# Performance work log

Hardware: AMD Instinct MI355X
Metric: run time of the kernel (lower is better)

Reference implementation:

```python
import jax, jax.numpy as jnp
import numpy as np

N = 100000   # nodes
E = 1600000  # edges
G = 256      # graphs in batch
IN = 128     # in_feats
H = 64       # h_feats


def _xavier(k, shape):
    fan_in, fan_out = shape
    lim = float(np.sqrt(6.0 / (fan_in + fan_out)))
    return jax.random.uniform(k, shape, jnp.float32, -lim, lim)


def setup_inputs() -> dict:
    key = jax.random.key(0)
    ks = jax.random.split(key, 12)
    x = jax.random.normal(ks[0], (N, IN), jnp.float32)
    src = jax.random.randint(ks[1], (E,), 0, N)
    dst = jax.random.randint(ks[2], (E,), 0, N)
    ew = jax.random.uniform(ks[3], (E,), jnp.float32)
    gid = jnp.sort(jax.random.randint(ks[4], (N,), 0, G))
    def lin(k, fi, fo):
        kw, kb = jax.random.split(k)
        lim = float(np.sqrt(1.0 / fi))
        return (jax.random.uniform(kw, (fi, fo), jnp.float32, -lim, lim),
                jax.random.uniform(kb, (fo,), jnp.float32, -lim, lim))
    W1 = _xavier(ks[5], (IN, H)); b1 = jnp.zeros((H,), jnp.float32)
    W2 = _xavier(ks[6], (H, H));  b2 = jnp.zeros((H,), jnp.float32)
    W3 = _xavier(ks[7], (H, H));  b3 = jnp.zeros((H,), jnp.float32)
    Dw1, Db1 = lin(ks[8], H, 16)
    Dw2, Db2 = lin(ks[9], 16, 8)
    Dw3, Db3 = lin(ks[10], 8, 1)
    return {"x": x, "src": src, "dst": dst, "ew": ew, "gid": gid,
            "W1": W1, "b1": b1, "W2": W2, "b2": b2, "W3": W3, "b3": b3,
            "Dw1": Dw1, "Db1": Db1, "Dw2": Dw2, "Db2": Db2, "Dw3": Dw3, "Db3": Db3}


def reference(x, src, dst, ew, gid, W1, b1, W2, b2, W3, b3,
              Dw1, Db1, Dw2, Db2, Dw3, Db3):
    n = x.shape[0]
    # DGL GraphConv norm='both': unweighted degrees, clamped to >= 1
    deg_out = jnp.zeros((n,), x.dtype).at[src].add(1.0)
    deg_in = jnp.zeros((n,), x.dtype).at[dst].add(1.0)
    ns = jax.lax.rsqrt(jnp.maximum(deg_out, 1.0))  # src-side norm
    nd = jax.lax.rsqrt(jnp.maximum(deg_in, 1.0))   # dst-side norm

    def conv(h, W, b):
        # apply weight first (in >= out), then gather-scale-scatter
        h = (h * ns[:, None]) @ W                      # [N, out]
        m = h[src] * ew[:, None]                       # [E, out] edge messages
        agg = jnp.zeros((n, W.shape[1]), h.dtype).at[dst].add(m)
        return agg * nd[:, None] + b

    h = jax.nn.relu(conv(x, W1, b1))
    h = jax.nn.relu(conv(h, W2, b2))
    h = jax.nn.relu(conv(h, W3, b3))

    # mean_nodes: per-graph mean pooling
    counts = jnp.zeros((G,), h.dtype).at[gid].add(1.0)
    pooled = jnp.zeros((G, h.shape[1]), h.dtype).at[gid].add(h)
    pooled = pooled / jnp.maximum(counts, 1.0)[:, None]

    h = jax.nn.relu(pooled @ Dw1 + Db1)
    h = jax.nn.relu(h @ Dw2 + Db2)
    return jax.nn.sigmoid(h @ Dw3 + Db3)  # [G, 1]
```

## Files before the change

kernel.cpp:

```cpp
#include <hip/hip_runtime.h>
#include <math.h>

#define N_NODES 100000
#define N_EDGES 1600000
#define G_GRAPHS 256
#define IN_F 128
#define H_F 64

#define HB 20
#define HCHUNK (N_EDGES / HB)
#define NWORDS (N_NODES / 4)
#define HNODES 25000
#define HWORDS (HNODES / 4)
#define HR 4

#define NREG 160
#define REG_NODES 625
#define BUCKET_CAP 11000
#define BSPAN 6400
#define NB_BUCKET (N_EDGES / BSPAN)
#define RSLACK 1280
#define STG_CAP 12880
#define CSR_ALLOC 1806336

typedef unsigned int uint_t;
typedef unsigned short ushort_t;
typedef unsigned char uchar_t;
typedef __attribute__((ext_vector_type(8))) short short8;
typedef __attribute__((ext_vector_type(4))) float floatx4;
typedef __attribute__((ext_vector_type(2))) float floatx2;

__device__ __forceinline__ ushort_t f2bf(float f) {
  uint_t u = __float_as_uint(f);
  uint_t r = (u + 0x7fffu + ((u >> 16) & 1u)) >> 16;
  return (ushort_t)r;
}
__device__ __forceinline__ float bflo(uint_t u) { return __uint_as_float(u << 16); }
__device__ __forceinline__ uchar_t f2fp8(float f) {
  return (uchar_t)(__builtin_amdgcn_cvt_pk_fp8_f32(f, f, 0, false) & 0xff);
}
__device__ __forceinline__ int sw_idx(int row, int kshort) {
  int slot = kshort >> 3;
  return row * 64 + (((slot ^ (row & 7)) << 3) | (kshort & 7));
}

__global__ __launch_bounds__(256) void build_a_kernel(
    const int* __restrict__ src, const int* __restrict__ dst,
    const float* __restrict__ ew, int* __restrict__ bcnt,
    uint2* __restrict__ bucket, uint_t* __restrict__ p8src) {
  __shared__ uint_t shm[BSPAN + 2 * NREG];
  if (blockIdx.x < NB_BUCKET) {
    uint_t* rl = shm;
    int* cnt = (int*)(shm + BSPAN);
    int* cur = cnt + NREG;
    const int e0 = blockIdx.x * BSPAN;

    for (int i = threadIdx.x; i < NREG; i += 256) cnt[i] = 0;
    __syncthreads();

    for (int i = threadIdx.x; i < BSPAN; i += 256) {
      uint_t d = (uint_t)dst[e0 + i];
      uint_t r = d / REG_NODES;
      uint_t loc = d - r * REG_NODES;
      rl[i] = (r << 16) | loc;
      atomicAdd(&cnt[r], 1);
    }
    __syncthreads();

    for (int i = threadIdx.x; i < NREG; i += 256)
      cur[i] = atomicAdd(&bcnt[i], cnt[i]);
    __syncthreads();

    for (int i = threadIdx.x; i < BSPAN; i += 256) {
      uint_t v = rl[i];
      uint_t r = v >> 16, loc = v & 0xffffu;
      int pos = atomicAdd(&cur[r], 1);
      if (pos < BUCKET_CAP)
        bucket[(size_t)r * BUCKET_CAP + pos] = make_uint2(
            (loc << 17) | (uint_t)src[e0 + i], __float_as_uint(ew[e0 + i]));
    }
  } else {
    uint_t* h = shm;
    const int idx = blockIdx.x - NB_BUCKET;
    const int r = idx / HB;
    const int b = idx % HB;
    const uint_t rbase = (uint_t)(r * HNODES);

    for (int i = threadIdx.x; i < HWORDS; i += 256) h[i] = 0u;
    __syncthreads();

    const uint4* k4 = (const uint4*)(src + b * HCHUNK);
    for (int i = threadIdx.x; i < HCHUNK / 4; i += 256) {
      uint4 v = k4[i];
      uint_t t;
      t = v.x - rbase; if (t < (uint_t)HNODES) atomicAdd(&h[t >> 2], 1u << ((t & 3u) * 8u));
      t = v.y - rbase; if (t < (uint_t)HNODES) atomicAdd(&h[t >> 2], 1u << ((t & 3u) * 8u));
      t = v.z - rbase; if (t < (uint_t)HNODES) atomicAdd(&h[t >> 2], 1u << ((t & 3u) * 8u));
      t = v.w - rbase; if (t < (uint_t)HNODES) atomicAdd(&h[t >> 2], 1u << ((t & 3u) * 8u));
    }
    __syncthreads();

    uint_t* outp = p8src + (size_t)b * NWORDS + r * HWORDS;
    for (int i = threadIdx.x; i < HWORDS; i += 256) outp[i] = h[i];
  }
}

__global__ __launch_bounds__(1024) void build_b_kernel(
    const uint2* __restrict__ bucket, const int* __restrict__ bcnt,
    const uint_t* __restrict__ p8src, uint_t* __restrict__ csr,
    int2* __restrict__ rc, float* __restrict__ nd, float* __restrict__ ns) {
  __shared__ uint_t staged[STG_CAP];
  __shared__ int cnt[REG_NODES];
  __shared__ int sc[REG_NODES];
  __shared__ int ts[1024];
  const int tid = threadIdx.x;
  if (blockIdx.x >= NREG) {
    int w = (blockIdx.x - NREG) * 1024 + tid;
    if (w >= NWORDS) return;
    int c0 = 0, c1 = 0, c2 = 0, c3 = 0;
    for (int b = 0; b < HB; ++b) {
      uint_t xv = p8src[(size_t)b * NWORDS + w];
      c0 += (int)(xv & 0xffu);
      c1 += (int)((xv >> 8) & 0xffu);
      c2 += (int)((xv >> 16) & 0xffu);
      c3 += (int)((xv >> 24) & 0xffu);
    }
    ((float4*)ns)[w] = make_float4(
        rsqrtf(fmaxf((float)c0, 1.0f)), rsqrtf(fmaxf((float)c1, 1.0f)),
        rsqrtf(fmaxf((float)c2, 1.0f)), rsqrtf(fmaxf((float)c3, 1.0f)));
    return;
  }
  const int r = blockIdx.x;
  const int nE = min(bcnt[r], BUCKET_CAP);
  const int alloc_r = ((nE + 3) & ~3) + RSLACK;

  ts[tid] = (tid < NREG) ? (((min(bcnt[tid], BUCKET_CAP) + 3) & ~3) + RSLACK) : 0;
  for (int i = tid; i < REG_NODES; i += 1024) cnt[i] = 0;
  __syncthreads();
  for (int off = 1; off < 256; off <<= 1) {
    int t = (tid >= off) ? ts[tid - off] : 0;
    __syncthreads();
    ts[tid] += t;
    __syncthreads();
  }
  const int csr_base = (r == 0) ? 0 : ts[r - 1];
  __syncthreads();

  const uint2* bk = bucket + (size_t)r * BUCKET_CAP;
  for (int i = tid; i < nE; i += 1024) atomicAdd(&cnt[bk[i].x >> 17], 1);
  __syncthreads();

  int cv = (tid < REG_NODES) ? cnt[tid] : 0;
  int pv = (cv + 3) & ~3;
  ts[tid] = pv;
  __syncthreads();
  for (int off = 1; off < 1024; off <<= 1) {
    int t = (tid >= off) ? ts[tid - off] : 0;
    __syncthreads();
    ts[tid] += t;
    __syncthreads();
  }
  if (tid < REG_NODES) {
    int run = (tid == 0) ? 0 : ts[tid - 1];
    sc[tid] = run;
    int v = r * REG_NODES + tid;
    rc[v] = make_int2(csr_base + run, cv);
    nd[v] = rsqrtf(fmaxf((float)cv, 1.0f));
  }
  __syncthreads();
  const int ptot = min(ts[1023], STG_CAP);
  __syncthreads();

  for (int i = tid; i < ptot; i += 1024) staged[i] = 0u;
  __syncthreads();

  for (int i = tid; i < nE; i += 1024) {
    uint2 e = bk[i];
    uint_t loc = e.x >> 17;
    int pos = atomicAdd(&sc[loc], 1);
    if (pos < STG_CAP)
      staged[pos] = ((uint_t)(f2bf(__uint_as_float(e.y)) & 0x7fff) << 17) |
                    (e.x & 0x1ffffu);
  }
  __syncthreads();

  const int out_len = min(ptot, alloc_r);
  for (int i = tid; i < out_len; i += 1024) csr[csr_base + i] = staged[i];
}

template <int K, bool AFP32>
__global__ __launch_bounds__(256) void gemm_mfma_kernel(
    const void* __restrict__ Xin, const float* __restrict__ W,
    const float* __restrict__ ns, uchar_t* __restrict__ T, int ntiles) {
  constexpr int CH = K / 32;
  constexpr int WROW = K + 8;
  __shared__ __align__(16) ushort_t Wt[64 * WROW];
  const int tid = threadIdx.x;

  for (int i = tid; i < K * 64; i += 256) {
    int k = i >> 6, nn = i & 63;
    Wt[nn * WROW + k] = f2bf(W[i]);
  }
  __syncthreads();

  const int wave = tid >> 6;
  const int lane = tid & 63;
  const int tile = blockIdx.x * 4 + wave;
  if (tile >= ntiles) return;
  const int m = lane & 15;
  const int q = lane >> 4;
  const int node0 = tile * 16;

  short8 afrag[CH];
  if (AFP32) {
    const float* xr = (const float*)Xin + (size_t)(node0 + m) * K + q * 8;
#pragma unroll
    for (int c = 0; c < CH; ++c) {
      float4 xa = *(const float4*)(xr + c * 32);
      float4 xb = *(const float4*)(xr + c * 32 + 4);
      short8 a;
      a[0] = (short)f2bf(xa.x); a[1] = (short)f2bf(xa.y);
      a[2] = (short)f2bf(xa.z); a[3] = (short)f2bf(xa.w);
      a[4] = (short)f2bf(xb.x); a[5] = (short)f2bf(xb.y);
      a[6] = (short)f2bf(xb.z); a[7] = (short)f2bf(xb.w);
      afrag[c] = a;
    }
  } else {
    const ushort_t* xr = (const ushort_t*)Xin + (size_t)(node0 + m) * K + q * 8;
#pragma unroll
    for (int c = 0; c < CH; ++c)
      afrag[c] = *(const short8*)(xr + c * 32);
  }

  floatx4 acc[4];
#pragma unroll
  for (int t = 0; t < 4; ++t) acc[t] = (floatx4){0.f, 0.f, 0.f, 0.f};

#pragma unroll
  for (int t = 0; t < 4; ++t) {
    const ushort_t* wr = &Wt[(t * 16 + m) * WROW + q * 8];
#pragma unroll
    for (int c = 0; c < CH; ++c) {
      short8 bfrag = *(const short8*)(wr + c * 32);
      acc[t] = __builtin_amdgcn_mfma_f32_16x16x32_bf16(afrag[c], bfrag, acc[t], 0, 0, 0);
    }
  }

  float4 nsv = *(const float4*)(ns + node0 + q * 4);
  const float nsa[4] = {nsv.x, nsv.y, nsv.z, nsv.w};
#pragma unroll
  for (int t = 0; t < 4; ++t) {
#pragma unroll
    for (int r = 0; r < 4; ++r) {
      int node = node0 + q * 4 + r;
      T[(size_t)node * 64 + t * 16 + m] = f2fp8(acc[t][r] * nsa[r]);
    }
  }
}

__device__ __forceinline__ void gacc1(float acc[8], uint_t e, uint2 p) {
  float w = __uint_as_float((e >> 17) << 16);
  floatx2 a;
  a = __builtin_amdgcn_cvt_pk_f32_fp8(p.x, false);
  acc[0] = fmaf(a.x, w, acc[0]); acc[1] = fmaf(a.y, w, acc[1]);
  a = __builtin_amdgcn_cvt_pk_f32_fp8(p.x, true);
  acc[2] = fmaf(a.x, w, acc[2]); acc[3] = fmaf(a.y, w, acc[3]);
  a = __builtin_amdgcn_cvt_pk_f32_fp8(p.y, false);
  acc[4] = fmaf(a.x, w, acc[4]); acc[5] = fmaf(a.y, w, acc[5]);
  a = __builtin_amdgcn_cvt_pk_f32_fp8(p.y, true);
  acc[6] = fmaf(a.x, w, acc[6]); acc[7] = fmaf(a.y, w, acc[7]);
}

template <bool POOL>
__global__ __launch_bounds__(256, 6) void fused_kernel(
    const uint_t* __restrict__ csr, const int2* __restrict__ rc,
    const uchar_t* __restrict__ T, const float* __restrict__ nd,
    const float* __restrict__ bias, const float* __restrict__ ns,
    const float* __restrict__ W, uchar_t* __restrict__ Tout,
    const int* __restrict__ gid, float* __restrict__ pooled) {
  __shared__ __align__(16) ushort_t Hs[POOL ? 8 : 64 * 64];
  __shared__ __align__(16) ushort_t Wt[POOL ? 8 : 64 * 64];
  __shared__ float gaccF[POOL ? 4 * 64 : 1];
  __shared__ int g0s;
  const int tid = threadIdx.x;
  const int node_base = blockIdx.x * 64;

  if constexpr (POOL) {
    gaccF[tid] = 0.0f;
    if (tid == 0) g0s = gid[node_base];
  } else {
    for (int i = tid; i < H_F * 64; i += 256) {
      int k = i >> 6, nn = i & 63;
      Wt[sw_idx(nn, k)] = f2bf(W[i]);
    }
  }
  __syncthreads();

  const int lane = tid & 63;
  const int wv = tid >> 6;
  const int o = lane >> 3, l = lane & 7;
  const uint2* Tp = (const uint2*)T;

  const float4 b0 = *(const float4*)&bias[l * 8];
  const float4 b1v = *(const float4*)&bias[l * 8 + 4];

#pragma unroll 1
  for (int pass = 0; pass < 2; ++pass) {
    const int ln = pass * 32 + wv * 8 + o;
    const int v = node_base + ln;
    if (v < N_NODES) {
      int2 rcv = rc[v];
      const uint4* c4 = (const uint4*)(csr + rcv.x);
      const int nb4 = (rcv.y + 3) >> 2;

      float acc[8] = {0, 0, 0, 0, 0, 0, 0, 0};
      int kq = 0;
      for (; kq + 2 <= nb4; kq += 2) {
        uint4 ea = c4[kq];
        uint4 eb = c4[kq + 1];
        uint2 p0 = Tp[(size_t)(ea.x & 0x1ffffu) * 8 + l];
        uint2 p1 = Tp[(size_t)(ea.y & 0x1ffffu) * 8 + l];
        uint2 p2 = Tp[(size_t)(ea.z & 0x1ffffu) * 8 + l];
        uint2 p3 = Tp[(size_t)(ea.w & 0x1ffffu) * 8 + l];
        uint2 p4 = Tp[(size_t)(eb.x & 0x1ffffu) * 8 + l];
        uint2 p5 = Tp[(size_t)(eb.y & 0x1ffffu) * 8 + l];
        uint2 p6 = Tp[(size_t)(eb.z & 0x1ffffu) * 8 + l];
        uint2 p7 = Tp[(size_t)(eb.w & 0x1ffffu) * 8 + l];
        gacc1(acc, ea.x, p0); gacc1(acc, ea.y, p1);
        gacc1(acc, ea.z, p2); gacc1(acc, ea.w, p3);
        gacc1(acc, eb.x, p4); gacc1(acc, eb.y, p5);
        gacc1(acc, eb.z, p6); gacc1(acc, eb.w, p7);
      }
      if (kq < nb4) {
        uint4 ea = c4[kq];
        uint2 p0 = Tp[(size_t)(ea.x & 0x1ffffu) * 8 + l];
        uint2 p1 = Tp[(size_t)(ea.y & 0x1ffffu) * 8 + l];
        uint2 p2 = Tp[(size_t)(ea.z & 0x1ffffu) * 8 + l];
        uint2 p3 = Tp[(size_t)(ea.w & 0x1ffffu) * 8 + l];
        gacc1(acc, ea.x, p0); gacc1(acc, ea.y, p1);
        gacc1(acc, ea.z, p2); gacc1(acc, ea.w, p3);
      }

      const float ndv = nd[v];
      if constexpr (!POOL) {
        uint4 ov;
        ov.x = (uint_t)f2bf(fmaxf(fmaf(acc[0], ndv, b0.x), 0.f)) |
               ((uint_t)f2bf(fmaxf(fmaf(acc[1], ndv, b0.y), 0.f)) << 16);
        ov.y = (uint_t)f2bf(fmaxf(fmaf(acc[2], ndv, b0.z), 0.f)) |
               ((uint_t)f2bf(fmaxf(fmaf(acc[3], ndv, b0.w), 0.f)) << 16);
        ov.z = (uint_t)f2bf(fmaxf(fmaf(acc[4], ndv, b1v.x), 0.f)) |
               ((uint_t)f2bf(fmaxf(fmaf(acc[5], ndv, b1v.y), 0.f)) << 16);
        ov.w = (uint_t)f2bf(fmaxf(fmaf(acc[6], ndv, b1v.z), 0.f)) |
               ((uint_t)f2bf(fmaxf(fmaf(acc[7], ndv, b1v.w), 0.f)) << 16);
        *((uint4*)&Hs[sw_idx(ln, l * 8)]) = ov;
      } else {
        const float bb[8] = {b0.x, b0.y, b0.z, b0.w, b1v.x, b1v.y, b1v.z, b1v.w};
        float vals[8];
#pragma unroll
        for (int f = 0; f < 8; ++f)
          vals[f] = bflo((uint_t)f2bf(fmaxf(fmaf(acc[f], ndv, bb[f]), 0.f)));
        int g = gid[v];
        int gl = g - g0s;
        if (gl >= 0 && gl < 4) {
#pragma unroll
          for (int f = 0; f < 8; ++f)
            atomicAdd(&gaccF[gl * 64 + l * 8 + f], vals[f]);
        } else {
#pragma unroll
          for (int f = 0; f < 8; ++f)
            atomicAdd(&pooled[(size_t)g * 64 + l * 8 + f], vals[f]);
        }
      }
    }
  }
  __syncthreads();

  if constexpr (!POOL) {
    const int m = lane & 15, q = lane >> 4;
    const int node0 = node_base + wv * 16;
    if (node0 < N_NODES) {
      short8 afrag[2];
      afrag[0] = *(const short8*)&Hs[sw_idx(wv * 16 + m, q * 8)];
      afrag[1] = *(const short8*)&Hs[sw_idx(wv * 16 + m, q * 8 + 32)];

      floatx4 acc4v[4];
#pragma unroll
      for (int t = 0; t < 4; ++t) acc4v[t] = (floatx4){0.f, 0.f, 0.f, 0.f};
#pragma unroll
      for (int t = 0; t < 4; ++t) {
#pragma unroll
        for (int c = 0; c < 2; ++c) {
          short8 bfrag = *(const short8*)&Wt[sw_idx(t * 16 + m, q * 8 + c * 32)];
          acc4v[t] = __builtin_amdgcn_mfma_f32_16x16x32_bf16(afrag[c], bfrag,
                                                            acc4v[t], 0, 0, 0);
        }
      }
      float4 nsv = *(const float4*)(ns + node0 + q * 4);
      const float nsa[4] = {nsv.x, nsv.y, nsv.z, nsv.w};
#pragma unroll
      for (int t = 0; t < 4; ++t) {
#pragma unroll
        for (int r2 = 0; r2 < 4; ++r2) {
          int node = node0 + q * 4 + r2;
          Tout[(size_t)node * 64 + t * 16 + m] = f2fp8(acc4v[t][r2] * nsa[r2]);
        }
      }
    }
  } else {
    int vlast = node_base + 63;
    if (vlast >= N_NODES) vlast = N_NODES - 1;
    int span = gid[vlast] - g0s + 1;
    if (span > 4) span = 4;
    if (tid < span * 64) {
      int gl = tid >> 6, j = tid & 63;
      int g = g0s + gl;
      if (g < G_GRAPHS) {
        float vsum = gaccF[gl * 64 + j];
        if (vsum != 0.0f) atomicAdd(&pooled[(size_t)g * 64 + j], vsum);
      }
    }
  }
}

__global__ __launch_bounds__(256) void pool_mlp_kernel(
    const float* __restrict__ pooled, const int* __restrict__ gid,
    const float* __restrict__ Dw1, const float* __restrict__ Db1,
    const float* __restrict__ Dw2, const float* __restrict__ Db2,
    const float* __restrict__ Dw3, const float* __restrict__ Db3,
    float* __restrict__ out) {
  __shared__ float mean[64];
  __shared__ float h1s[16], h2s[8];
  const int g = blockIdx.x;
  int l = 0, r = N_NODES;
  while (l < r) { int m = (l + r) >> 1; if (gid[m] < g) l = m + 1; else r = m; }
  const int lo = l;
  r = N_NODES;
  while (l < r) { int m = (l + r) >> 1; if (gid[m] < g + 1) l = m + 1; else r = m; }
  const int hi = l;

  if (threadIdx.x < 64) {
    float inv = 1.0f / fmaxf((float)(hi - lo), 1.0f);
    mean[threadIdx.x] = pooled[(size_t)g * 64 + threadIdx.x] * inv;
  }
  __syncthreads();
  if (threadIdx.x < 16) {
    int o = threadIdx.x;
    float a = Db1[o];
#pragma unroll
    for (int k = 0; k < 64; ++k) a = fmaf(mean[k], Dw1[k * 16 + o], a);
    h1s[o] = fmaxf(a, 0.0f);
  }
  __syncthreads();
  if (threadIdx.x < 8) {
    int o = threadIdx.x;
    float a = Db2[o];
#pragma unroll
    for (int k = 0; k < 16; ++k) a = fmaf(h1s[k], Dw2[k * 8 + o], a);
    h2s[o] = fmaxf(a, 0.0f);
  }
  __syncthreads();
  if (threadIdx.x == 0) {
    float a = Db3[0];
#pragma unroll
    for (int k = 0; k < 8; ++k) a = fmaf(h2s[k], Dw3[k], a);
    out[g] = 1.0f / (1.0f + expf(-a));
  }
}

extern "C" void kernel_launch(void* const* d_in, const int* in_sizes, int n_in,
                              void* d_out, int out_size, void* d_ws, size_t ws_size,
                              hipStream_t stream) {
  const float* x   = (const float*)d_in[0];
  const int*   src = (const int*)  d_in[1];
  const int*   dst = (const int*)  d_in[2];
  const float* ew  = (const float*)d_in[3];
  const int*   gid = (const int*)  d_in[4];
  const float* W1  = (const float*)d_in[5];
  const float* b1  = (const float*)d_in[6];
  const float* W2  = (const float*)d_in[7];
  const float* b2  = (const float*)d_in[8];
  const float* W3  = (const float*)d_in[9];
  const float* b3  = (const float*)d_in[10];
  const float* Dw1 = (const float*)d_in[11];
  const float* Db1 = (const float*)d_in[12];
  const float* Dw2 = (const float*)d_in[13];
  const float* Db2 = (const float*)d_in[14];
  const float* Dw3 = (const float*)d_in[15];
  const float* Db3 = (const float*)d_in[16];
  float* out = (float*)d_out;

  char* ws = (char*)d_ws;
  const size_t TSZ = (size_t)N_NODES * 64;
  const size_t BUCKET_BYTES = (size_t)NREG * BUCKET_CAP * 8;
  uchar_t*  T_a   = (uchar_t*)ws;
  uchar_t*  T_b   = (uchar_t*)(ws + TSZ);
  uint2*    bucket = (uint2*)ws;
  char* p = ws + BUCKET_BYTES;
  uint_t*   csr   = (uint_t*)p;          p += (size_t)CSR_ALLOC * 4;
  uint_t*   p8src = (uint_t*)p;          p += (size_t)HB * NWORDS * 4;
  float*    ns    = (float*)p;           p += (size_t)N_NODES * 4;
  float*    nd    = (float*)p;           p += (size_t)N_NODES * 4;
  int2*     rc    = (int2*)p;            p += (size_t)N_NODES * 8;
  int*      bcnt  = (int*)p;             p += (size_t)NREG * 4;
  float*    pooled = (float*)p;

  const int NTILES  = N_NODES / 16;
  const int NB_A    = NB_BUCKET + HR * HB;
  const int NB_B    = NREG + (NWORDS + 1023) / 1024;
  const int NB_GEMM = (NTILES + 3) / 4;
  const int NB_F    = (N_NODES + 63) / 64;

  hipMemsetAsync(bcnt, 0,
                 NREG * sizeof(int) + G_GRAPHS * H_F * sizeof(float), stream);
  build_a_kernel<<<NB_A, 256, 0, stream>>>(src, dst, ew, bcnt, bucket, p8src);
  build_b_kernel<<<NB_B, 1024, 0, stream>>>(bucket, bcnt, p8src, csr, rc, nd, ns);

  gemm_mfma_kernel<IN_F, true><<<NB_GEMM, 256, 0, stream>>>(x, W1, ns, T_a, NTILES);
  fused_kernel<false><<<NB_F, 256, 0, stream>>>(csr, rc, T_a, nd, b1, ns, W2,
                                                T_b, nullptr, nullptr);
  fused_kernel<false><<<NB_F, 256, 0, stream>>>(csr, rc, T_b, nd, b2, ns, W3,
                                                T_a, nullptr, nullptr);
  fused_kernel<true><<<NB_F, 256, 0, stream>>>(csr, rc, T_a, nd, b3, nullptr,
                                               nullptr, nullptr, gid, pooled);

  pool_mlp_kernel<<<G_GRAPHS, 256, 0, stream>>>(pooled, gid, Dw1, Db1, Dw2, Db2,
                                                Dw3, Db3, out);
}
```

Before: 289.2 us.

## Switch aggregation to edge-balanced work split with packed CSR and LDS accumulation

The per-node aggregation loop is replaced with an edge-parallel scheme. Each block walks the contiguous edge range of its 64 nodes. Octets of lanes process 8 edges each, receive edge descriptors through ds_bpermute, and flush run-length partial sums into an LDS accumulator with atomics. The CSR drops the per-node padding to multiples of 4 and gains a byte array holding each edge's local destination index. The aim is to remove load imbalance from skewed degrees and the wasted padding traffic, at the cost of LDS atomics, an extra byte stream per edge, and lower occupancy (launch bound 4 instead of 6).

```diff
diff --git a/kernel.cpp b/kernel.cpp
--- a/kernel.cpp
+++ b/kernel.cpp
@@ -19,9 +19,7 @@
 #define BUCKET_CAP 11000
 #define BSPAN 6400
 #define NB_BUCKET (N_EDGES / BSPAN)
-#define RSLACK 1280
-#define STG_CAP 12880
-#define CSR_ALLOC 1806336
+#define CSR_SLACK 512
 
 typedef unsigned int uint_t;
 typedef unsigned short ushort_t;
@@ -108,8 +106,10 @@
 __global__ __launch_bounds__(1024) void build_b_kernel(
     const uint2* __restrict__ bucket, const int* __restrict__ bcnt,
     const uint_t* __restrict__ p8src, uint_t* __restrict__ csr,
-    int2* __restrict__ rc, float* __restrict__ nd, float* __restrict__ ns) {
-  __shared__ uint_t staged[STG_CAP];
+    uchar_t* __restrict__ locb, int2* __restrict__ rc,
+    float* __restrict__ nd, float* __restrict__ ns) {
+  __shared__ uint_t staged[BUCKET_CAP];
+  __shared__ uchar_t stagedb[BUCKET_CAP];
   __shared__ int cnt[REG_NODES];
   __shared__ int sc[REG_NODES];
   __shared__ int ts[1024];
@@ -132,9 +132,8 @@
   }
   const int r = blockIdx.x;
   const int nE = min(bcnt[r], BUCKET_CAP);
-  const int alloc_r = ((nE + 3) & ~3) + RSLACK;
-
-  ts[tid] = (tid < NREG) ? (((min(bcnt[tid], BUCKET_CAP) + 3) & ~3) + RSLACK) : 0;
+
+  ts[tid] = (tid < NREG) ? min(bcnt[tid], BUCKET_CAP) : 0;
   for (int i = tid; i < REG_NODES; i += 1024) cnt[i] = 0;
   __syncthreads();
   for (int off = 1; off < 256; off <<= 1) {
@@ -151,8 +150,7 @@
   __syncthreads();
 
   int cv = (tid < REG_NODES) ? cnt[tid] : 0;
-  int pv = (cv + 3) & ~3;
-  ts[tid] = pv;
+  ts[tid] = cv;
   __syncthreads();
   for (int off = 1; off < 1024; off <<= 1) {
     int t = (tid >= off) ? ts[tid - off] : 0;
@@ -168,24 +166,21 @@
     nd[v] = rsqrtf(fmaxf((float)cv, 1.0f));
   }
   __syncthreads();
-  const int ptot = min(ts[1023], STG_CAP);
-  __syncthreads();
-
-  for (int i = tid; i < ptot; i += 1024) staged[i] = 0u;
-  __syncthreads();
 
   for (int i = tid; i < nE; i += 1024) {
     uint2 e = bk[i];
     uint_t loc = e.x >> 17;
     int pos = atomicAdd(&sc[loc], 1);
-    if (pos < STG_CAP)
-      staged[pos] = ((uint_t)(f2bf(__uint_as_float(e.y)) & 0x7fff) << 17) |
-                    (e.x & 0x1ffffu);
-  }
-  __syncthreads();
-
-  const int out_len = min(ptot, alloc_r);
-  for (int i = tid; i < out_len; i += 1024) csr[csr_base + i] = staged[i];
+    staged[pos] = ((uint_t)(f2bf(__uint_as_float(e.y)) & 0x7fff) << 17) |
+                  (e.x & 0x1ffffu);
+    stagedb[pos] = (uchar_t)(((uint_t)r * REG_NODES + loc) & 63u);
+  }
+  __syncthreads();
+
+  for (int i = tid; i < nE; i += 1024) {
+    csr[csr_base + i] = staged[i];
+    locb[csr_base + i] = stagedb[i];
+  }
 }
 
 template <int K, bool AFP32>
@@ -258,33 +253,23 @@
   }
 }
 
-__device__ __forceinline__ void gacc1(float acc[8], uint_t e, uint2 p) {
-  float w = __uint_as_float((e >> 17) << 16);
-  floatx2 a;
-  a = __builtin_amdgcn_cvt_pk_f32_fp8(p.x, false);
-  acc[0] = fmaf(a.x, w, acc[0]); acc[1] = fmaf(a.y, w, acc[1]);
-  a = __builtin_amdgcn_cvt_pk_f32_fp8(p.x, true);
-  acc[2] = fmaf(a.x, w, acc[2]); acc[3] = fmaf(a.y, w, acc[3]);
-  a = __builtin_amdgcn_cvt_pk_f32_fp8(p.y, false);
-  acc[4] = fmaf(a.x, w, acc[4]); acc[5] = fmaf(a.y, w, acc[5]);
-  a = __builtin_amdgcn_cvt_pk_f32_fp8(p.y, true);
-  acc[6] = fmaf(a.x, w, acc[6]); acc[7] = fmaf(a.y, w, acc[7]);
-}
-
 template <bool POOL>
-__global__ __launch_bounds__(256, 6) void fused_kernel(
-    const uint_t* __restrict__ csr, const int2* __restrict__ rc,
-    const uchar_t* __restrict__ T, const float* __restrict__ nd,
-    const float* __restrict__ bias, const float* __restrict__ ns,
-    const float* __restrict__ W, uchar_t* __restrict__ Tout,
-    const int* __restrict__ gid, float* __restrict__ pooled) {
-  __shared__ __align__(16) ushort_t Hs[POOL ? 8 : 64 * 64];
+__global__ __launch_bounds__(256, 4) void fused_kernel(
+    const uint_t* __restrict__ csr, const uchar_t* __restrict__ locb,
+    const int2* __restrict__ rc, const uchar_t* __restrict__ T,
+    const float* __restrict__ nd, const float* __restrict__ bias,
+    const float* __restrict__ ns, const float* __restrict__ W,
+    uchar_t* __restrict__ Tout, const int* __restrict__ gid,
+    float* __restrict__ pooled) {
+  __shared__ float Hacc[64 * 65];
   __shared__ __align__(16) ushort_t Wt[POOL ? 8 : 64 * 64];
-  __shared__ float gaccF[POOL ? 4 * 64 : 1];
+  __shared__ float gaccF[POOL ? 256 : 1];
   __shared__ int g0s;
   const int tid = threadIdx.x;
   const int node_base = blockIdx.x * 64;
-
+  const int vlast = min(node_base + 63, N_NODES - 1);
+
+  for (int i = tid; i < 64 * 65; i += 256) Hacc[i] = 0.0f;
   if constexpr (POOL) {
     gaccF[tid] = 0.0f;
     if (tid == 0) g0s = gid[node_base];
@@ -299,78 +284,73 @@
   const int lane = tid & 63;
   const int wv = tid >> 6;
   const int o = lane >> 3, l = lane & 7;
+  const int oct = wv * 8 + o;
   const uint2* Tp = (const uint2*)T;
 
-  const float4 b0 = *(const float4*)&bias[l * 8];
-  const float4 b1v = *(const float4*)&bias[l * 8 + 4];
-
-#pragma unroll 1
-  for (int pass = 0; pass < 2; ++pass) {
-    const int ln = pass * 32 + wv * 8 + o;
-    const int v = node_base + ln;
-    if (v < N_NODES) {
-      int2 rcv = rc[v];
-      const uint4* c4 = (const uint4*)(csr + rcv.x);
-      const int nb4 = (rcv.y + 3) >> 2;
-
-      float acc[8] = {0, 0, 0, 0, 0, 0, 0, 0};
-      int kq = 0;
-      for (; kq + 2 <= nb4; kq += 2) {
-        uint4 ea = c4[kq];
-        uint4 eb = c4[kq + 1];
-        uint2 p0 = Tp[(size_t)(ea.x & 0x1ffffu) * 8 + l];
-        uint2 p1 = Tp[(size_t)(ea.y & 0x1ffffu) * 8 + l];
-        uint2 p2 = Tp[(size_t)(ea.z & 0x1ffffu) * 8 + l];
-        uint2 p3 = Tp[(size_t)(ea.w & 0x1ffffu) * 8 + l];
-        uint2 p4 = Tp[(size_t)(eb.x & 0x1ffffu) * 8 + l];
-        uint2 p5 = Tp[(size_t)(eb.y & 0x1ffffu) * 8 + l];
-        uint2 p6 = Tp[(size_t)(eb.z & 0x1ffffu) * 8 + l];
-        uint2 p7 = Tp[(size_t)(eb.w & 0x1ffffu) * 8 + l];
-        gacc1(acc, ea.x, p0); gacc1(acc, ea.y, p1);
-        gacc1(acc, ea.z, p2); gacc1(acc, ea.w, p3);
-        gacc1(acc, eb.x, p4); gacc1(acc, eb.y, p5);
-        gacc1(acc, eb.z, p6); gacc1(acc, eb.w, p7);
+  const int2 rc0 = rc[node_base];
+  const int2 rcL = rc[vlast];
+  const int ws = rc0.x;
+  const int we = rcL.x + rcL.y;
+
+  float acc[8] = {0, 0, 0, 0, 0, 0, 0, 0};
+  int loc_run = -1;
+
+  int eb = ws + oct * 8;
+  if (eb < we) {
+    uint_t dl = csr[eb + l];
+    uint_t bl = (uint_t)locb[eb + l];
+    for (; eb < we; eb += 256) {
+      uint_t dln = csr[eb + 256 + l];
+      uint_t bln = (uint_t)locb[eb + 256 + l];
+
+      uint_t descs[8];
+      int locs[8];
+#pragma unroll
+      for (int j = 0; j < 8; ++j) {
+        const int idx4 = (((lane & 56) | j) << 2);
+        descs[j] = (uint_t)__builtin_amdgcn_ds_bpermute(idx4, (int)dl);
+        locs[j] = __builtin_amdgcn_ds_bpermute(idx4, (int)bl);
       }
-      if (kq < nb4) {
-        uint4 ea = c4[kq];
-        uint2 p0 = Tp[(size_t)(ea.x & 0x1ffffu) * 8 + l];
-        uint2 p1 = Tp[(size_t)(ea.y & 0x1ffffu) * 8 + l];
-        uint2 p2 = Tp[(size_t)(ea.z & 0x1ffffu) * 8 + l];
-        uint2 p3 = Tp[(size_t)(ea.w & 0x1ffffu) * 8 + l];
-        gacc1(acc, ea.x, p0); gacc1(acc, ea.y, p1);
-        gacc1(acc, ea.z, p2); gacc1(acc, ea.w, p3);
-      }
-
-      const float ndv = nd[v];
-      if constexpr (!POOL) {
-        uint4 ov;
-        ov.x = (uint_t)f2bf(fmaxf(fmaf(acc[0], ndv, b0.x), 0.f)) |
-               ((uint_t)f2bf(fmaxf(fmaf(acc[1], ndv, b0.y), 0.f)) << 16);
-        ov.y = (uint_t)f2bf(fmaxf(fmaf(acc[2], ndv, b0.z), 0.f)) |
-               ((uint_t)f2bf(fmaxf(fmaf(acc[3], ndv, b0.w), 0.f)) << 16);
-        ov.z = (uint_t)f2bf(fmaxf(fmaf(acc[4], ndv, b1v.x), 0.f)) |
-               ((uint_t)f2bf(fmaxf(fmaf(acc[5], ndv, b1v.y), 0.f)) << 16);
-        ov.w = (uint_t)f2bf(fmaxf(fmaf(acc[6], ndv, b1v.z), 0.f)) |
-               ((uint_t)f2bf(fmaxf(fmaf(acc[7], ndv, b1v.w), 0.f)) << 16);
-        *((uint4*)&Hs[sw_idx(ln, l * 8)]) = ov;
-      } else {
-        const float bb[8] = {b0.x, b0.y, b0.z, b0.w, b1v.x, b1v.y, b1v.z, b1v.w};
-        float vals[8];
-#pragma unroll
-        for (int f = 0; f < 8; ++f)
-          vals[f] = bflo((uint_t)f2bf(fmaxf(fmaf(acc[f], ndv, bb[f]), 0.f)));
-        int g = gid[v];
-        int gl = g - g0s;
-        if (gl >= 0 && gl < 4) {
-#pragma unroll
-          for (int f = 0; f < 8; ++f)
-            atomicAdd(&gaccF[gl * 64 + l * 8 + f], vals[f]);
-        } else {
-#pragma unroll
-          for (int f = 0; f < 8; ++f)
-            atomicAdd(&pooled[(size_t)g * 64 + l * 8 + f], vals[f]);
+      uint2 p[8];
+#pragma unroll
+      for (int j = 0; j < 8; ++j)
+        p[j] = Tp[(size_t)(descs[j] & 0x1ffffu) * 8 + l];
+
+      const int nrem = we - eb;
+#pragma unroll
+      for (int j = 0; j < 8; ++j) {
+        if (j < nrem) {
+          const int lj = locs[j];
+          if (lj != loc_run) {
+            if (loc_run >= 0) {
+              float* hb = &Hacc[loc_run * 65 + l * 8];
+#pragma unroll
+              for (int f = 0; f < 8; ++f) {
+                atomicAdd(&hb[f], acc[f]);
+                acc[f] = 0.0f;
+              }
+            }
+            loc_run = lj;
+          }
+          const float w = __uint_as_float((descs[j] >> 17) << 16);
+          floatx2 a;
+          a = __builtin_amdgcn_cvt_pk_f32_fp8(p[j].x, false);
+          acc[0] = fmaf(a.x, w, acc[0]); acc[1] = fmaf(a.y, w, acc[1]);
+          a = __builtin_amdgcn_cvt_pk_f32_fp8(p[j].x, true);
+          acc[2] = fmaf(a.x, w, acc[2]); acc[3] = fmaf(a.y, w, acc[3]);
+          a = __builtin_amdgcn_cvt_pk_f32_fp8(p[j].y, false);
+          acc[4] = fmaf(a.x, w, acc[4]); acc[5] = fmaf(a.y, w, acc[5]);
+          a = __builtin_amdgcn_cvt_pk_f32_fp8(p[j].y, true);
+          acc[6] = fmaf(a.x, w, acc[6]); acc[7] = fmaf(a.y, w, acc[7]);
         }
       }
+      dl = dln;
+      bl = bln;
+    }
+    if (loc_run >= 0) {
+      float* hb = &Hacc[loc_run * 65 + l * 8];
+#pragma unroll
+      for (int f = 0; f < 8; ++f) atomicAdd(&hb[f], acc[f]);
     }
   }
   __syncthreads();
@@ -379,9 +359,23 @@
     const int m = lane & 15, q = lane >> 4;
     const int node0 = node_base + wv * 16;
     if (node0 < N_NODES) {
+      const int v = node0 + m;
+      const float ndv = nd[v];
+      const float* hr = &Hacc[(wv * 16 + m) * 65 + q * 8];
+      float4 bq0 = *(const float4*)&bias[q * 8];
+      float4 bq1 = *(const float4*)&bias[q * 8 + 4];
+      float4 bq2 = *(const float4*)&bias[q * 8 + 32];
+      float4 bq3 = *(const float4*)&bias[q * 8 + 36];
+      const float ba[16] = {bq0.x, bq0.y, bq0.z, bq0.w, bq1.x, bq1.y, bq1.z,
+                            bq1.w, bq2.x, bq2.y, bq2.z, bq2.w, bq3.x, bq3.y,
+                            bq3.z, bq3.w};
       short8 afrag[2];
-      afrag[0] = *(const short8*)&Hs[sw_idx(wv * 16 + m, q * 8)];
-      afrag[1] = *(const short8*)&Hs[sw_idx(wv * 16 + m, q * 8 + 32)];
+#pragma unroll
+      for (int f = 0; f < 8; ++f)
+        afrag[0][f] = (short)f2bf(fmaxf(fmaf(hr[f], ndv, ba[f]), 0.0f));
+#pragma unroll
+      for (int f = 0; f < 8; ++f)
+        afrag[1][f] = (short)f2bf(fmaxf(fmaf(hr[32 + f], ndv, ba[8 + f]), 0.0f));
 
       floatx4 acc4v[4];
 #pragma unroll
@@ -407,8 +401,24 @@
       }
     }
   } else {
-    int vlast = node_base + 63;
-    if (vlast >= N_NODES) vlast = N_NODES - 1;
+    const int feat = tid & 63;
+    const float bf = bias[feat];
+#pragma unroll
+    for (int k = 0; k < 16; ++k) {
+      const int row = (tid >> 6) + k * 4;
+      const int v = node_base + row;
+      if (v < N_NODES) {
+        float val = bflo((uint_t)f2bf(
+            fmaxf(fmaf(Hacc[row * 65 + feat], nd[v], bf), 0.0f)));
+        const int g = gid[v];
+        const int gl = g - g0s;
+        if (gl >= 0 && gl < 4)
+          atomicAdd(&gaccF[gl * 64 + feat], val);
+        else
+          atomicAdd(&pooled[(size_t)g * 64 + feat], val);
+      }
+    }
+    __syncthreads();
     int span = gid[vlast] - g0s + 1;
     if (span > 4) span = 4;
     if (tid < span * 64) {
@@ -496,7 +506,8 @@
   uchar_t*  T_b   = (uchar_t*)(ws + TSZ);
   uint2*    bucket = (uint2*)ws;
   char* p = ws + BUCKET_BYTES;
-  uint_t*   csr   = (uint_t*)p;          p += (size_t)CSR_ALLOC * 4;
+  uint_t*   csr   = (uint_t*)p;          p += (size_t)(N_EDGES + CSR_SLACK) * 4;
+  uchar_t*  locb  = (uchar_t*)p;         p += (size_t)(N_EDGES + CSR_SLACK);
   uint_t*   p8src = (uint_t*)p;          p += (size_t)HB * NWORDS * 4;
   float*    ns    = (float*)p;           p += (size_t)N_NODES * 4;
   float*    nd    = (float*)p;           p += (size_t)N_NODES * 4;
@@ -513,15 +524,17 @@
   hipMemsetAsync(bcnt, 0,
                  NREG * sizeof(int) + G_GRAPHS * H_F * sizeof(float), stream);
   build_a_kernel<<<NB_A, 256, 0, stream>>>(src, dst, ew, bcnt, bucket, p8src);
-  build_b_kernel<<<NB_B, 1024, 0, stream>>>(bucket, bcnt, p8src, csr, rc, nd, ns);
+  build_b_kernel<<<NB_B, 1024, 0, stream>>>(bucket, bcnt, p8src, csr, locb,
+                                            rc, nd, ns);
 
   gemm_mfma_kernel<IN_F, true><<<NB_GEMM, 256, 0, stream>>>(x, W1, ns, T_a, NTILES);
-  fused_kernel<false><<<NB_F, 256, 0, stream>>>(csr, rc, T_a, nd, b1, ns, W2,
-                                                T_b, nullptr, nullptr);
-  fused_kernel<false><<<NB_F, 256, 0, stream>>>(csr, rc, T_b, nd, b2, ns, W3,
-                                                T_a, nullptr, nullptr);
-  fused_kernel<true><<<NB_F, 256, 0, stream>>>(csr, rc, T_a, nd, b3, nullptr,
-                                               nullptr, nullptr, gid, pooled);
+  fused_kernel<false><<<NB_F, 256, 0, stream>>>(csr, locb, rc, T_a, nd, b1, ns,
+                                                W2, T_b, nullptr, nullptr);
+  fused_kernel<false><<<NB_F, 256, 0, stream>>>(csr, locb, rc, T_b, nd, b2, ns,
+                                                W3, T_a, nullptr, nullptr);
+  fused_kernel<true><<<NB_F, 256, 0, stream>>>(csr, locb, rc, T_a, nd, b3,
+                                               nullptr, nullptr, nullptr, gid,
+                                               pooled);
 
   pool_mlp_kernel<<<G_GRAPHS, 256, 0, stream>>>(pooled, gid, Dw1, Db1, Dw2, Db2,
                                                 Dw3, Db3, out);
```

After: 572.1 us. 97.8% more time.

## Pack CSR tightly and sort each node's edges by source quarter

Applied to the files above, without the earlier changes.

The CSR build stops padding each node's neighbour list to a multiple of four with zero entries plus per-region slack, and lays it out densely. Within each destination node, edges are now grouped into four buckets by source-node range, so neighbour gathers touch nearer addresses in T and may hit cache more often. The aggregation loop switches from aligned uint4 CSR loads to scalar loads with a remainder loop. This removes the wasted padded-edge gathers and the zero-fill, at the cost of unaligned, narrower index loads and a slightly more expensive bucketing pass with a division per edge.

```diff
diff --git a/kernel.cpp b/kernel.cpp
--- a/kernel.cpp
+++ b/kernel.cpp
@@ -19,9 +19,8 @@
 #define BUCKET_CAP 11000
 #define BSPAN 6400
 #define NB_BUCKET (N_EDGES / BSPAN)
-#define RSLACK 1280
-#define STG_CAP 12880
-#define CSR_ALLOC 1806336
+#define NQ 4
+#define QDIV 25000
 
 typedef unsigned int uint_t;
 typedef unsigned short ushort_t;
@@ -109,9 +108,9 @@
     const uint2* __restrict__ bucket, const int* __restrict__ bcnt,
     const uint_t* __restrict__ p8src, uint_t* __restrict__ csr,
     int2* __restrict__ rc, float* __restrict__ nd, float* __restrict__ ns) {
-  __shared__ uint_t staged[STG_CAP];
-  __shared__ int cnt[REG_NODES];
-  __shared__ int sc[REG_NODES];
+  __shared__ uint_t staged[BUCKET_CAP];
+  __shared__ int cnt4[REG_NODES * NQ];
+  __shared__ int sc4[REG_NODES * NQ];
   __shared__ int ts[1024];
   const int tid = threadIdx.x;
   if (blockIdx.x >= NREG) {
@@ -132,10 +131,9 @@
   }
   const int r = blockIdx.x;
   const int nE = min(bcnt[r], BUCKET_CAP);
-  const int alloc_r = ((nE + 3) & ~3) + RSLACK;
-
-  ts[tid] = (tid < NREG) ? (((min(bcnt[tid], BUCKET_CAP) + 3) & ~3) + RSLACK) : 0;
-  for (int i = tid; i < REG_NODES; i += 1024) cnt[i] = 0;
+
+  ts[tid] = (tid < NREG) ? min(bcnt[tid], BUCKET_CAP) : 0;
+  for (int i = tid; i < REG_NODES * NQ; i += 1024) cnt4[i] = 0;
   __syncthreads();
   for (int off = 1; off < 256; off <<= 1) {
     int t = (tid >= off) ? ts[tid - off] : 0;
@@ -147,12 +145,20 @@
   __syncthreads();
 
   const uint2* bk = bucket + (size_t)r * BUCKET_CAP;
-  for (int i = tid; i < nE; i += 1024) atomicAdd(&cnt[bk[i].x >> 17], 1);
-  __syncthreads();
-
-  int cv = (tid < REG_NODES) ? cnt[tid] : 0;
-  int pv = (cv + 3) & ~3;
-  ts[tid] = pv;
+  for (int i = tid; i < nE; i += 1024) {
+    uint_t ex = bk[i].x;
+    uint_t loc = ex >> 17;
+    uint_t q = (ex & 0x1ffffu) / QDIV;
+    atomicAdd(&cnt4[loc * NQ + q], 1);
+  }
+  __syncthreads();
+
+  int c4[NQ], cv = 0;
+  if (tid < REG_NODES) {
+#pragma unroll
+    for (int q = 0; q < NQ; ++q) { c4[q] = cnt4[tid * NQ + q]; cv += c4[q]; }
+  }
+  ts[tid] = (tid < REG_NODES) ? cv : 0;
   __syncthreads();
   for (int off = 1; off < 1024; off <<= 1) {
     int t = (tid >= off) ? ts[tid - off] : 0;
@@ -162,30 +168,25 @@
   }
   if (tid < REG_NODES) {
     int run = (tid == 0) ? 0 : ts[tid - 1];
-    sc[tid] = run;
     int v = r * REG_NODES + tid;
     rc[v] = make_int2(csr_base + run, cv);
     nd[v] = rsqrtf(fmaxf((float)cv, 1.0f));
-  }
-  __syncthreads();
-  const int ptot = min(ts[1023], STG_CAP);
-  __syncthreads();
-
-  for (int i = tid; i < ptot; i += 1024) staged[i] = 0u;
+#pragma unroll
+    for (int q = 0; q < NQ; ++q) { sc4[tid * NQ + q] = run; run += c4[q]; }
+  }
   __syncthreads();
 
   for (int i = tid; i < nE; i += 1024) {
     uint2 e = bk[i];
     uint_t loc = e.x >> 17;
-    int pos = atomicAdd(&sc[loc], 1);
-    if (pos < STG_CAP)
-      staged[pos] = ((uint_t)(f2bf(__uint_as_float(e.y)) & 0x7fff) << 17) |
-                    (e.x & 0x1ffffu);
-  }
-  __syncthreads();
-
-  const int out_len = min(ptot, alloc_r);
-  for (int i = tid; i < out_len; i += 1024) csr[csr_base + i] = staged[i];
+    uint_t q = (e.x & 0x1ffffu) / QDIV;
+    int pos = atomicAdd(&sc4[loc * NQ + q], 1);
+    staged[pos] = ((uint_t)(f2bf(__uint_as_float(e.y)) & 0x7fff) << 17) |
+                  (e.x & 0x1ffffu);
+  }
+  __syncthreads();
+
+  for (int i = tid; i < nE; i += 1024) csr[csr_base + i] = staged[i];
 }
 
 template <int K, bool AFP32>
@@ -280,10 +281,11 @@
     const int* __restrict__ gid, float* __restrict__ pooled) {
   __shared__ __align__(16) ushort_t Hs[POOL ? 8 : 64 * 64];
   __shared__ __align__(16) ushort_t Wt[POOL ? 8 : 64 * 64];
-  __shared__ float gaccF[POOL ? 4 * 64 : 1];
+  __shared__ float gaccF[POOL ? 256 : 1];
   __shared__ int g0s;
   const int tid = threadIdx.x;
   const int node_base = blockIdx.x * 64;
+  const int vlast = min(node_base + 63, N_NODES - 1);
 
   if constexpr (POOL) {
     gaccF[tid] = 0.0f;
@@ -310,35 +312,23 @@
     const int v = node_base + ln;
     if (v < N_NODES) {
       int2 rcv = rc[v];
-      const uint4* c4 = (const uint4*)(csr + rcv.x);
-      const int nb4 = (rcv.y + 3) >> 2;
-
+      int k = rcv.x;
+      const int ke = rcv.x + rcv.y;
       float acc[8] = {0, 0, 0, 0, 0, 0, 0, 0};
-      int kq = 0;
-      for (; kq + 2 <= nb4; kq += 2) {
-        uint4 ea = c4[kq];
-        uint4 eb = c4[kq + 1];
-        uint2 p0 = Tp[(size_t)(ea.x & 0x1ffffu) * 8 + l];
-        uint2 p1 = Tp[(size_t)(ea.y & 0x1ffffu) * 8 + l];
-        uint2 p2 = Tp[(size_t)(ea.z & 0x1ffffu) * 8 + l];
-        uint2 p3 = Tp[(size_t)(ea.w & 0x1ffffu) * 8 + l];
-        uint2 p4 = Tp[(size_t)(eb.x & 0x1ffffu) * 8 + l];
-        uint2 p5 = Tp[(size_t)(eb.y & 0x1ffffu) * 8 + l];
-        uint2 p6 = Tp[(size_t)(eb.z & 0x1ffffu) * 8 + l];
-        uint2 p7 = Tp[(size_t)(eb.w & 0x1ffffu) * 8 + l];
-        gacc1(acc, ea.x, p0); gacc1(acc, ea.y, p1);
-        gacc1(acc, ea.z, p2); gacc1(acc, ea.w, p3);
-        gacc1(acc, eb.x, p4); gacc1(acc, eb.y, p5);
-        gacc1(acc, eb.z, p6); gacc1(acc, eb.w, p7);
+
+      for (; k + 4 <= ke; k += 4) {
+        uint_t e0 = csr[k], e1 = csr[k + 1], e2 = csr[k + 2], e3 = csr[k + 3];
+        uint2 p0 = Tp[(size_t)(e0 & 0x1ffffu) * 8 + l];
+        uint2 p1 = Tp[(size_t)(e1 & 0x1ffffu) * 8 + l];
+        uint2 p2 = Tp[(size_t)(e2 & 0x1ffffu) * 8 + l];
+        uint2 p3 = Tp[(size_t)(e3 & 0x1ffffu) * 8 + l];
+        gacc1(acc, e0, p0); gacc1(acc, e1, p1);
+        gacc1(acc, e2, p2); gacc1(acc, e3, p3);
       }
-      if (kq < nb4) {
-        uint4 ea = c4[kq];
-        uint2 p0 = Tp[(size_t)(ea.x & 0x1ffffu) * 8 + l];
-        uint2 p1 = Tp[(size_t)(ea.y & 0x1ffffu) * 8 + l];
-        uint2 p2 = Tp[(size_t)(ea.z & 0x1ffffu) * 8 + l];
-        uint2 p3 = Tp[(size_t)(ea.w & 0x1ffffu) * 8 + l];
-        gacc1(acc, ea.x, p0); gacc1(acc, ea.y, p1);
-        gacc1(acc, ea.z, p2); gacc1(acc, ea.w, p3);
+      for (; k < ke; ++k) {
+        uint_t e0 = csr[k];
+        uint2 p0 = Tp[(size_t)(e0 & 0x1ffffu) * 8 + l];
+        gacc1(acc, e0, p0);
       }
 
       const float ndv = nd[v];
@@ -407,8 +397,6 @@
       }
     }
   } else {
-    int vlast = node_base + 63;
-    if (vlast >= N_NODES) vlast = N_NODES - 1;
     int span = gid[vlast] - g0s + 1;
     if (span > 4) span = 4;
     if (tid < span * 64) {
@@ -496,7 +484,7 @@
   uchar_t*  T_b   = (uchar_t*)(ws + TSZ);
   uint2*    bucket = (uint2*)ws;
   char* p = ws + BUCKET_BYTES;
-  uint_t*   csr   = (uint_t*)p;          p += (size_t)CSR_ALLOC * 4;
+  uint_t*   csr   = (uint_t*)p;          p += (size_t)N_EDGES * 4;
   uint_t*   p8src = (uint_t*)p;          p += (size_t)HB * NWORDS * 4;
   float*    ns    = (float*)p;           p += (size_t)N_NODES * 4;
   float*    nd    = (float*)p;           p += (size_t)N_NODES * 4;
```

Result: slower. 314.4 us (+8.7%).
